# Performance work log

Measured on AMD Instinct MI355X. Metric: run time of the kernel, lower is better.

The kernel has to match this reference:

```python
import jax, jax.numpy as jnp
import numpy as np

N_HEAD = 16  # matches init_kwargs
LN_EPS = 1e-5


def setup_inputs() -> dict:
    key = jax.random.key(0)
    k0, k1, k2 = jax.random.split(key, 3)
    S, B, D = 2048, 2, 1024
    N, Dh = N_HEAD, D // N_HEAD
    h = jax.random.normal(k0, (S, B, D), dtype=jnp.float32)
    # causal mask, True = masked; source's dim==3 branch: shape [qlen, klen, batch]
    causal = jnp.triu(jnp.ones((S, S), dtype=bool), k=1)
    attn_mask = jnp.broadcast_to(causal[:, :, None], (S, S, B))
    W_qkv = jax.random.normal(k1, (D, 3 * N * Dh), dtype=jnp.float32) * (1.0 / np.sqrt(D))
    W_o = jax.random.normal(k2, (N * Dh, D), dtype=jnp.float32) * (1.0 / np.sqrt(N * Dh))
    gamma = jnp.ones((D,), dtype=jnp.float32)
    beta = jnp.zeros((D,), dtype=jnp.float32)
    return {"h": h, "attn_mask": attn_mask, "W_qkv": W_qkv, "W_o": W_o,
            "gamma": gamma, "beta": beta}


def reference(h, attn_mask, W_qkv, W_o, gamma, beta):
    # h: [S, B, D] (seq, batch, d_model) -- Transformer-XL layout
    S, B, D = h.shape
    N = N_HEAD
    Dh = W_o.shape[0] // N
    scale = 1.0 / np.sqrt(Dh)

    qkv = h @ W_qkv                                   # [S, B, 3*N*Dh]
    q, k, v = jnp.split(qkv, 3, axis=-1)
    q = q.reshape(S, B, N, Dh)
    k = k.reshape(S, B, N, Dh)
    v = v.reshape(S, B, N, Dh)

    # attention scores: [i, j, b, n]
    score = jnp.einsum('ibnd,jbnd->ijbn', q, k) * scale
    # mask (dim==3 branch of source): attn_mask [i, j, b] -> [i, j, b, 1]
    score = jnp.where(attn_mask[:, :, :, None], -jnp.inf, score)
    prob = jax.nn.softmax(score, axis=1)              # softmax over key axis j

    attn_vec = jnp.einsum('ijbn,jbnd->ibnd', prob, v).reshape(S, B, N * Dh)
    attn_out = attn_vec @ W_o                         # [S, B, D]

    # residual + LayerNorm (biased variance, like torch.nn.LayerNorm)
    x = h + attn_out
    mu = jnp.mean(x, axis=-1, keepdims=True)
    var = jnp.mean(jnp.square(x - mu), axis=-1, keepdims=True)
    out = (x - mu) * jax.lax.rsqrt(var + LN_EPS) * gamma + beta
    return out
```

## Files before the change

### kernel.cpp

```cpp
#include <hip/hip_runtime.h>

typedef unsigned short u16;
typedef unsigned int u32;
typedef __attribute__((ext_vector_type(8))) __bf16 bf16x8;
typedef __attribute__((ext_vector_type(4))) float f32x4;
typedef __attribute__((ext_vector_type(8))) unsigned short u16x8;
typedef __attribute__((ext_vector_type(4))) unsigned short u16x4;

__device__ __forceinline__ u16 f2bf(float f) {
    u32 u = __builtin_bit_cast(u32, f);
    u += 0x7fffu + ((u >> 16) & 1u);
    return (u16)(u >> 16);
}

__device__ __forceinline__ float fexp2(float x) {
#if __has_builtin(__builtin_amdgcn_exp2f)
    return __builtin_amdgcn_exp2f(x);
#else
    return exp2f(x);
#endif
}

__device__ __forceinline__ float frcp(float x) {
#if __has_builtin(__builtin_amdgcn_rcpf)
    return __builtin_amdgcn_rcpf(x);
#else
    return 1.0f / x;
#endif
}

__global__ __launch_bounds__(256) void conv_h_kernel(const float* __restrict__ h,
                                                     u16* __restrict__ hb) {
    int i = blockIdx.x * 256 + threadIdx.x;
    float4 v = ((const float4*)h)[i];
    u16x4 o = { f2bf(v.x), f2bf(v.y), f2bf(v.z), f2bf(v.w) };
    ((u16x4*)hb)[i] = o;
}

__global__ __launch_bounds__(256) void conv_wt_kernel(const float* __restrict__ W,
                                                      u16* __restrict__ Wt,
                                                      int R, int C,
                                                      int scale_rows, float scale) {
    __shared__ float tile[32][33];
    int t = threadIdx.x;
    int r = t >> 3, c4 = (t & 7) * 4;
    int gx = blockIdx.x * 32, gy = blockIdx.y * 32;
    float4 v = *(const float4*)&W[(size_t)(gy + r) * C + gx + c4];
    tile[r][c4 + 0] = v.x; tile[r][c4 + 1] = v.y;
    tile[r][c4 + 2] = v.z; tile[r][c4 + 3] = v.w;
    __syncthreads();
    float sc = (gx + r < scale_rows) ? scale : 1.0f;
    u16x4 o = { f2bf(tile[c4 + 0][r] * sc), f2bf(tile[c4 + 1][r] * sc),
                f2bf(tile[c4 + 2][r] * sc), f2bf(tile[c4 + 3][r] * sc) };
    *(u16x4*)&Wt[(size_t)(gx + r) * R + gy + c4] = o;
}

template <int MODE>
__global__ __launch_bounds__(256) void gemm_bt_kernel(
        const u16* __restrict__ A, const u16* __restrict__ Bt,
        u16* __restrict__ Cb, const float* __restrict__ H, float* __restrict__ X,
        int M, int N, int K) {
    constexpr int LDT = 40;
    __shared__ u16 alds[2][128 * LDT];
    __shared__ u16 blds[2][128 * LDT];
    const int t = threadIdx.x;
    const int lane = t & 63;
    const int wave = t >> 6;
    const int wm = wave >> 1, wn = wave & 1;
    const int m0 = blockIdx.x * 128;
    const int n0 = blockIdx.y * 128;
    const int nk = K >> 5;

    const int srow = t >> 1;
    const int sch = (t & 1) * 2;
    const u16* ga = A + (size_t)(m0 + srow) * K + sch * 8;
    const u16* gb = Bt + (size_t)(n0 + srow) * K + sch * 8;
    const int wo = srow * LDT + sch * 8;

    u16x8 ra0 = *(const u16x8*)(ga);
    u16x8 ra1 = *(const u16x8*)(ga + 8);
    u16x8 rb0 = *(const u16x8*)(gb);
    u16x8 rb1 = *(const u16x8*)(gb + 8);
    *(u16x8*)&alds[0][wo] = ra0;  *(u16x8*)&alds[0][wo + 8] = ra1;
    *(u16x8*)&blds[0][wo] = rb0;  *(u16x8*)&blds[0][wo + 8] = rb1;

    f32x4 acc[4][4] = {};
    const int ko = (lane >> 4) * 8;
    const int arow_base = wm * 64 + (lane & 15);
    const int brow_base = wn * 64 + (lane & 15);

    int cur = 0;
    for (int kt = 0; kt < nk; ++kt) {
        __syncthreads();
        if (kt + 1 < nk) {
            const u16* gan = ga + (kt + 1) * 32;
            const u16* gbn = gb + (kt + 1) * 32;
            ra0 = *(const u16x8*)(gan);
            ra1 = *(const u16x8*)(gan + 8);
            rb0 = *(const u16x8*)(gbn);
            rb1 = *(const u16x8*)(gbn + 8);
        }
        bf16x8 afrag[4], bfrag[4];
#pragma unroll
        for (int m = 0; m < 4; ++m)
            afrag[m] = *(const bf16x8*)&alds[cur][(arow_base + m * 16) * LDT + ko];
#pragma unroll
        for (int n = 0; n < 4; ++n)
            bfrag[n] = *(const bf16x8*)&blds[cur][(brow_base + n * 16) * LDT + ko];
#pragma unroll
        for (int m = 0; m < 4; ++m)
#pragma unroll
            for (int n = 0; n < 4; ++n)
                acc[m][n] = __builtin_amdgcn_mfma_f32_16x16x32_bf16(afrag[m], bfrag[n],
                                                                   acc[m][n], 0, 0, 0);
        if (kt + 1 < nk) {
            *(u16x8*)&alds[cur ^ 1][wo] = ra0;  *(u16x8*)&alds[cur ^ 1][wo + 8] = ra1;
            *(u16x8*)&blds[cur ^ 1][wo] = rb0;  *(u16x8*)&blds[cur ^ 1][wo + 8] = rb1;
        }
        cur ^= 1;
    }

#pragma unroll
    for (int m = 0; m < 4; ++m)
#pragma unroll
        for (int n = 0; n < 4; ++n)
#pragma unroll
            for (int r = 0; r < 4; ++r) {
                int row = m0 + wm * 64 + m * 16 + (lane >> 4) * 4 + r;
                int col = n0 + wn * 64 + n * 16 + (lane & 15);
                size_t idx = (size_t)row * N + col;
                if (MODE == 0) Cb[idx] = f2bf(acc[m][n][r]);
                else           X[idx] = acc[m][n][r] + H[idx];
            }
}

__global__ __launch_bounds__(256) void transpose_v_kernel(const u16* __restrict__ qkvb,
                                                          u16* __restrict__ vt) {
    __shared__ u16 tl[64][72];
    const int t = threadIdx.x;
    const int p = blockIdx.y;
    const int nn = p >> 1, b = p & 1;
    const int s0 = blockIdx.x * 64;
    const int r = t >> 2;
    const int ch = (t & 3) * 2;
    const u16* g = qkvb + ((size_t)(s0 + r) * 2 + b) * 3072 + 2048 + nn * 64;
    *(u16x8*)&tl[r][ch * 8]     = *(const u16x8*)(g + ch * 8);
    *(u16x8*)&tl[r][ch * 8 + 8] = *(const u16x8*)(g + ch * 8 + 8);
    __syncthreads();
    const int dh = t >> 2;
    const int sc = (t & 3) * 2;
    u16* o = vt + ((size_t)p * 64 + dh) * 2048 + s0;
#pragma unroll
    for (int q = 0; q < 2; ++q) {
        int scq = sc + q;
        u16x8 v;
#pragma unroll
        for (int j = 0; j < 8; ++j) v[j] = tl[scq * 8 + j][dh];
        *(u16x8*)(o + scq * 8) = v;
    }
}

__global__ __launch_bounds__(256) void attn_kernel(const u16* __restrict__ qkvb,
                                                   const u16* __restrict__ vt,
                                                   u16* __restrict__ attnb) {
    constexpr int LKT = 72;
    __shared__ u16 klds[64 * LKT];
    __shared__ u16 vlds[64 * LKT];
    __shared__ u16 plds[4][16 * LKT];
    const int t = threadIdx.x;
    const int lane = t & 63;
    const int w = t >> 6;
    const int bid = blockIdx.x;
    const int qt = 31 - (bid >> 5);
    const int p = bid & 31;
    const int nn = p >> 1, b = p & 1;
    const int i0 = qt * 64;

    const int li = lane & 15;
    const int lg = lane >> 4;

    const int qrow = i0 + w * 16 + li;
    const u16* qg = qkvb + ((size_t)qrow * 2 + b) * 3072 + nn * 64 + lg * 8;
    bf16x8 qa0 = *(const bf16x8*)(qg);
    bf16x8 qa1 = *(const bf16x8*)(qg + 32);

    f32x4 o[4] = {};
    float mrun = -3.0e38f;
    float lrun = 0.f;

    const int srow = t >> 2;
    const int sch = (t & 3) * 2;
    const u16* kg = qkvb + 1024 + nn * 64 + sch * 8;
    const u16* vg = vt + ((size_t)p * 64 + srow) * 2048 + sch * 8;

    const int nt = qt + 1;
    u16x8 k0, k1, v0, v1;
    {
        const u16* kgp = kg + ((size_t)srow * 2 + b) * 3072;
        k0 = *(const u16x8*)(kgp);  k1 = *(const u16x8*)(kgp + 8);
        v0 = *(const u16x8*)(vg);   v1 = *(const u16x8*)(vg + 8);
    }
    for (int jt = 0; jt < nt; ++jt) {
        const int j0 = jt * 64;
        __syncthreads();
        *(u16x8*)&klds[srow * LKT + sch * 8] = k0;
        *(u16x8*)&klds[srow * LKT + sch * 8 + 8] = k1;
        *(u16x8*)&vlds[srow * LKT + sch * 8] = v0;
        *(u16x8*)&vlds[srow * LKT + sch * 8 + 8] = v1;
        if (jt + 1 < nt) {
            const u16* kgp = kg + ((size_t)(j0 + 64 + srow) * 2 + b) * 3072;
            k0 = *(const u16x8*)(kgp);  k1 = *(const u16x8*)(kgp + 8);
            const u16* vgp = vg + j0 + 64;
            v0 = *(const u16x8*)(vgp);  v1 = *(const u16x8*)(vgp + 8);
        }
        __syncthreads();

        f32x4 st[4];
#pragma unroll
        for (int cf = 0; cf < 4; ++cf) {
            bf16x8 kb0 = *(const bf16x8*)&klds[(cf * 16 + li) * LKT + lg * 8];
            bf16x8 kb1 = *(const bf16x8*)&klds[(cf * 16 + li) * LKT + 32 + lg * 8];
            f32x4 z = {};
            z = __builtin_amdgcn_mfma_f32_16x16x32_bf16(kb0, qa0, z, 0, 0, 0);
            z = __builtin_amdgcn_mfma_f32_16x16x32_bf16(kb1, qa1, z, 0, 0, 0);
            st[cf] = z;
        }

        if (jt == qt) {
            const int it = w * 16 + li;
#pragma unroll
            for (int cf = 0; cf < 4; ++cf)
#pragma unroll
                for (int r = 0; r < 4; ++r) {
                    int jl = cf * 16 + lg * 4 + r;
                    if (jl > it) st[cf][r] = -3.0e38f;
                }
        }

        float mloc = st[0][0];
#pragma unroll
        for (int cf = 0; cf < 4; ++cf)
#pragma unroll
            for (int r = 0; r < 4; ++r) mloc = fmaxf(mloc, st[cf][r]);
        mloc = fmaxf(mloc, __shfl_xor(mloc, 16, 64));
        mloc = fmaxf(mloc, __shfl_xor(mloc, 32, 64));

        if (__any(mloc > mrun + 8.0f)) {
            float mnew = fmaxf(mrun, mloc);
            float alpha = fexp2(mrun - mnew);
            lrun *= alpha;
            mrun = mnew;
#pragma unroll
            for (int r = 0; r < 4; ++r) {
                float ar = __shfl(alpha, lg * 4 + r, 64);
#pragma unroll
                for (int cf = 0; cf < 4; ++cf) o[cf][r] *= ar;
            }
        }

        float rsum = 0.f;
#pragma unroll
        for (int cf = 0; cf < 4; ++cf) {
            u16x4 pw;
#pragma unroll
            for (int r = 0; r < 4; ++r) {
                float pv = fexp2(st[cf][r] - mrun);
                rsum += pv;
                pw[r] = f2bf(pv);
            }
            *(u16x4*)&plds[w][li * LKT + cf * 16 + lg * 4] = pw;
        }
        rsum += __shfl_xor(rsum, 16, 64);
        rsum += __shfl_xor(rsum, 32, 64);
        lrun += rsum;

        asm volatile("s_waitcnt lgkmcnt(0)" ::: "memory");
        __builtin_amdgcn_sched_barrier(0);

#pragma unroll
        for (int ks = 0; ks < 2; ++ks) {
            bf16x8 pa = *(const bf16x8*)&plds[w][li * LKT + ks * 32 + lg * 8];
#pragma unroll
            for (int cf = 0; cf < 4; ++cf) {
                bf16x8 vb = *(const bf16x8*)&vlds[(cf * 16 + li) * LKT + ks * 32 + lg * 8];
                o[cf] = __builtin_amdgcn_mfma_f32_16x16x32_bf16(pa, vb, o[cf], 0, 0, 0);
            }
        }
    }

    float rinv = frcp(lrun);
#pragma unroll
    for (int r = 0; r < 4; ++r) {
        float rv = __shfl(rinv, lg * 4 + r, 64);
        int srowg = i0 + w * 16 + lg * 4 + r;
        u16* og = attnb + ((size_t)srowg * 2 + b) * 1024 + nn * 64;
#pragma unroll
        for (int cf = 0; cf < 4; ++cf)
            og[cf * 16 + li] = f2bf(o[cf][r] * rv);
    }
}

__global__ __launch_bounds__(256) void ln_kernel(const float* __restrict__ X,
                                                 const float* __restrict__ gamma,
                                                 const float* __restrict__ beta,
                                                 float* __restrict__ out) {
    __shared__ float red[8];
    const int t = threadIdx.x;
    const int row = blockIdx.x;
    float4 v = ((const float4*)(X + (size_t)row * 1024))[t];
    float s = v.x + v.y + v.z + v.w;
#pragma unroll
    for (int off = 1; off < 64; off <<= 1) s += __shfl_xor(s, off, 64);
    if ((t & 63) == 0) red[t >> 6] = s;
    __syncthreads();
    float mu = (red[0] + red[1] + red[2] + red[3]) * (1.f / 1024.f);
    float dx = v.x - mu, dy = v.y - mu, dz = v.z - mu, dw = v.w - mu;
    float q = dx * dx + dy * dy + dz * dz + dw * dw;
#pragma unroll
    for (int off = 1; off < 64; off <<= 1) q += __shfl_xor(q, off, 64);
    if ((t & 63) == 0) red[4 + (t >> 6)] = q;
    __syncthreads();
    float var = (red[4] + red[5] + red[6] + red[7]) * (1.f / 1024.f);
    float rs = rsqrtf(var + 1e-5f);
    float4 g = ((const float4*)gamma)[t];
    float4 bt = ((const float4*)beta)[t];
    float4 o;
    o.x = dx * rs * g.x + bt.x;
    o.y = dy * rs * g.y + bt.y;
    o.z = dz * rs * g.z + bt.z;
    o.w = dw * rs * g.w + bt.w;
    ((float4*)(out + (size_t)row * 1024))[t] = o;
}

extern "C" void kernel_launch(void* const* d_in, const int* in_sizes, int n_in,
                              void* d_out, int out_size, void* d_ws, size_t ws_size,
                              hipStream_t stream) {
    const float* h     = (const float*)d_in[0];
    const float* Wqkv  = (const float*)d_in[2];
    const float* Wo    = (const float*)d_in[3];
    const float* gamma = (const float*)d_in[4];
    const float* beta  = (const float*)d_in[5];
    float* out = (float*)d_out;

    char* ws = (char*)d_ws;
    u16*   hb    = (u16*)(ws);
    u16*   wqkvt = (u16*)(ws + 8388608);
    u16*   wot   = (u16*)(ws + 14680064);
    u16*   qkvb  = (u16*)(ws + 16777216);
    u16*   vt    = (u16*)(ws + 41943040);
    u16*   attnb = (u16*)(ws + 50331648);
    float* xbuf  = (float*)(ws + 58720256);

    const float qscale = 0.125f * 1.44269504088896f;

    conv_h_kernel<<<4096, 256, 0, stream>>>(h, hb);
    conv_wt_kernel<<<dim3(96, 32), 256, 0, stream>>>(Wqkv, wqkvt, 1024, 3072, 1024, qscale);
    conv_wt_kernel<<<dim3(32, 32), 256, 0, stream>>>(Wo, wot, 1024, 1024, 0, 1.0f);
    gemm_bt_kernel<0><<<dim3(32, 24), 256, 0, stream>>>(hb, wqkvt, qkvb, nullptr, nullptr,
                                                        4096, 3072, 1024);
    transpose_v_kernel<<<dim3(32, 32), 256, 0, stream>>>(qkvb, vt);
    attn_kernel<<<1024, 256, 0, stream>>>(qkvb, vt, attnb);
    gemm_bt_kernel<1><<<dim3(32, 8), 256, 0, stream>>>(attnb, wot, nullptr, h, xbuf,
                                                       4096, 1024, 1024);
    ln_kernel<<<4096, 256, 0, stream>>>(xbuf, gamma, beta, out);
}
```

Before: 122.7 us.

## Use direct global-to-LDS loads in GEMM and 128-row query tiles in attention

The GEMM now stages A and B tiles with global_load_lds straight into unpadded shared memory, dropping the register round trip, with a wait and barrier after each k step. The attention kernel processes 128 query rows per block (two 16-row sub-blocks per wave), so each loaded K/V tile is reused twice as much, with half the grid and a reordered tile schedule. The work buys fewer LDS staging instructions and less K/V traffic, but costs unpadded LDS rows that may cause bank conflicts, more registers per wave, and fewer blocks in flight.

Result: slower. 132.5 us (+7.9%).

```diff
diff --git a/kernel.cpp b/kernel.cpp
--- a/kernel.cpp
+++ b/kernel.cpp
@@ -28,6 +28,10 @@
     return 1.0f / x;
 #endif
 }
+
+#define GLOAD_LDS16(gp, lp) __builtin_amdgcn_global_load_lds(                    \
+    (const __attribute__((address_space(1))) void*)(gp),                          \
+    (__attribute__((address_space(3))) void*)(lp), 16, 0, 0)
 
 __global__ __launch_bounds__(256) void conv_h_kernel(const float* __restrict__ h,
                                                      u16* __restrict__ hb) {
@@ -60,63 +64,62 @@
         const u16* __restrict__ A, const u16* __restrict__ Bt,
         u16* __restrict__ Cb, const float* __restrict__ H, float* __restrict__ X,
         int M, int N, int K) {
-    constexpr int LDT = 40;
-    __shared__ u16 alds[2][128 * LDT];
-    __shared__ u16 blds[2][128 * LDT];
+    __shared__ u16 alds[2][128 * 32];
+    __shared__ u16 blds[2][128 * 32];
     const int t = threadIdx.x;
     const int lane = t & 63;
     const int wave = t >> 6;
     const int wm = wave >> 1, wn = wave & 1;
+    const int li = lane & 15, lg = lane >> 4;
     const int m0 = blockIdx.x * 128;
     const int n0 = blockIdx.y * 128;
     const int nk = K >> 5;
 
-    const int srow = t >> 1;
-    const int sch = (t & 1) * 2;
-    const u16* ga = A + (size_t)(m0 + srow) * K + sch * 8;
-    const u16* gb = Bt + (size_t)(n0 + srow) * K + sch * 8;
-    const int wo = srow * LDT + sch * 8;
-
-    u16x8 ra0 = *(const u16x8*)(ga);
-    u16x8 ra1 = *(const u16x8*)(ga + 8);
-    u16x8 rb0 = *(const u16x8*)(gb);
-    u16x8 rb1 = *(const u16x8*)(gb + 8);
-    *(u16x8*)&alds[0][wo] = ra0;  *(u16x8*)&alds[0][wo + 8] = ra1;
-    *(u16x8*)&blds[0][wo] = rb0;  *(u16x8*)&blds[0][wo + 8] = rb1;
+    const int srow0 = (lane >> 2);
+    const int scol = (lane & 3) * 8;
+    const u16* gA = A + (size_t)(m0 + srow0) * K + scol;
+    const u16* gB = Bt + (size_t)(n0 + srow0) * K + scol;
+
+#define GEMM_STAGE(cur, kt)                                                      \
+    {                                                                            \
+        _Pragma("unroll")                                                        \
+        for (int jj = 0; jj < 2; ++jj) {                                         \
+            const int instr = wave * 2 + jj;                                     \
+            GLOAD_LDS16(gA + (size_t)(instr * 16) * K + (kt) * 32,               \
+                        &alds[cur][instr * 512]);                                \
+            GLOAD_LDS16(gB + (size_t)(instr * 16) * K + (kt) * 32,               \
+                        &blds[cur][instr * 512]);                                \
+        }                                                                        \
+    }
+
+    GEMM_STAGE(0, 0);
 
     f32x4 acc[4][4] = {};
-    const int ko = (lane >> 4) * 8;
-    const int arow_base = wm * 64 + (lane & 15);
-    const int brow_base = wn * 64 + (lane & 15);
+    const int ko = lg * 8;
+    const int arow_base = wm * 64 + li;
+    const int brow_base = wn * 64 + li;
+
+    asm volatile("s_waitcnt vmcnt(0)" ::: "memory");
+    __syncthreads();
 
     int cur = 0;
     for (int kt = 0; kt < nk; ++kt) {
-        __syncthreads();
-        if (kt + 1 < nk) {
-            const u16* gan = ga + (kt + 1) * 32;
-            const u16* gbn = gb + (kt + 1) * 32;
-            ra0 = *(const u16x8*)(gan);
-            ra1 = *(const u16x8*)(gan + 8);
-            rb0 = *(const u16x8*)(gbn);
-            rb1 = *(const u16x8*)(gbn + 8);
-        }
+        if (kt + 1 < nk) GEMM_STAGE(cur ^ 1, kt + 1);
         bf16x8 afrag[4], bfrag[4];
 #pragma unroll
         for (int m = 0; m < 4; ++m)
-            afrag[m] = *(const bf16x8*)&alds[cur][(arow_base + m * 16) * LDT + ko];
+            afrag[m] = *(const bf16x8*)&alds[cur][(arow_base + m * 16) * 32 + ko];
 #pragma unroll
         for (int n = 0; n < 4; ++n)
-            bfrag[n] = *(const bf16x8*)&blds[cur][(brow_base + n * 16) * LDT + ko];
+            bfrag[n] = *(const bf16x8*)&blds[cur][(brow_base + n * 16) * 32 + ko];
 #pragma unroll
         for (int m = 0; m < 4; ++m)
 #pragma unroll
             for (int n = 0; n < 4; ++n)
                 acc[m][n] = __builtin_amdgcn_mfma_f32_16x16x32_bf16(afrag[m], bfrag[n],
                                                                    acc[m][n], 0, 0, 0);
-        if (kt + 1 < nk) {
-            *(u16x8*)&alds[cur ^ 1][wo] = ra0;  *(u16x8*)&alds[cur ^ 1][wo + 8] = ra1;
-            *(u16x8*)&blds[cur ^ 1][wo] = rb0;  *(u16x8*)&blds[cur ^ 1][wo + 8] = rb1;
-        }
+        asm volatile("s_waitcnt vmcnt(0)" ::: "memory");
+        __syncthreads();
         cur ^= 1;
     }
 
@@ -126,8 +129,8 @@
         for (int n = 0; n < 4; ++n)
 #pragma unroll
             for (int r = 0; r < 4; ++r) {
-                int row = m0 + wm * 64 + m * 16 + (lane >> 4) * 4 + r;
-                int col = n0 + wn * 64 + n * 16 + (lane & 15);
+                int row = m0 + wm * 64 + m * 16 + lg * 4 + r;
+                int col = n0 + wn * 64 + n * 16 + li;
                 size_t idx = (size_t)row * N + col;
                 if (MODE == 0) Cb[idx] = f2bf(acc[m][n][r]);
                 else           X[idx] = acc[m][n][r] + H[idx];
@@ -166,34 +169,39 @@
     constexpr int LKT = 72;
     __shared__ u16 klds[64 * LKT];
     __shared__ u16 vlds[64 * LKT];
-    __shared__ u16 plds[4][16 * LKT];
+    __shared__ u16 plds[4][32 * LKT];
     const int t = threadIdx.x;
     const int lane = t & 63;
     const int w = t >> 6;
     const int bid = blockIdx.x;
-    const int qt = 31 - (bid >> 5);
+    const int g = bid >> 5;
+    const int qt = (g < 8) ? (15 - g) : (g - 8);
     const int p = bid & 31;
     const int nn = p >> 1, b = p & 1;
-    const int i0 = qt * 64;
+    const int i0 = qt * 128;
 
     const int li = lane & 15;
     const int lg = lane >> 4;
 
-    const int qrow = i0 + w * 16 + li;
-    const u16* qg = qkvb + ((size_t)qrow * 2 + b) * 3072 + nn * 64 + lg * 8;
-    bf16x8 qa0 = *(const bf16x8*)(qg);
-    bf16x8 qa1 = *(const bf16x8*)(qg + 32);
-
-    f32x4 o[4] = {};
-    float mrun = -3.0e38f;
-    float lrun = 0.f;
+    bf16x8 qa[2][2];
+#pragma unroll
+    for (int ib = 0; ib < 2; ++ib) {
+        const u16* qg = qkvb + ((size_t)(i0 + w * 32 + ib * 16 + li) * 2 + b) * 3072
+                        + nn * 64 + lg * 8;
+        qa[ib][0] = *(const bf16x8*)(qg);
+        qa[ib][1] = *(const bf16x8*)(qg + 32);
+    }
+
+    f32x4 o[4][2] = {};
+    float mrun[2] = { -3.0e38f, -3.0e38f };
+    float lrun[2] = { 0.f, 0.f };
 
     const int srow = t >> 2;
     const int sch = (t & 3) * 2;
     const u16* kg = qkvb + 1024 + nn * 64 + sch * 8;
     const u16* vg = vt + ((size_t)p * 64 + srow) * 2048 + sch * 8;
 
-    const int nt = qt + 1;
+    const int nt = 2 * qt + 2;
     u16x8 k0, k1, v0, v1;
     {
         const u16* kgp = kg + ((size_t)srow * 2 + b) * 3072;
@@ -215,89 +223,124 @@
         }
         __syncthreads();
 
-        f32x4 st[4];
-#pragma unroll
-        for (int cf = 0; cf < 4; ++cf) {
-            bf16x8 kb0 = *(const bf16x8*)&klds[(cf * 16 + li) * LKT + lg * 8];
-            bf16x8 kb1 = *(const bf16x8*)&klds[(cf * 16 + li) * LKT + 32 + lg * 8];
-            f32x4 z = {};
-            z = __builtin_amdgcn_mfma_f32_16x16x32_bf16(kb0, qa0, z, 0, 0, 0);
-            z = __builtin_amdgcn_mfma_f32_16x16x32_bf16(kb1, qa1, z, 0, 0, 0);
-            st[cf] = z;
+        const bool active = !(w < 2 && jt == nt - 1);
+        if (active) {
+            f32x4 st[4][2];
+#pragma unroll
+            for (int cf = 0; cf < 4; ++cf) {
+                bf16x8 kb0 = *(const bf16x8*)&klds[(cf * 16 + li) * LKT + lg * 8];
+                bf16x8 kb1 = *(const bf16x8*)&klds[(cf * 16 + li) * LKT + 32 + lg * 8];
+#pragma unroll
+                for (int ib = 0; ib < 2; ++ib) {
+                    f32x4 z = {};
+                    z = __builtin_amdgcn_mfma_f32_16x16x32_bf16(kb0, qa[ib][0], z, 0, 0, 0);
+                    z = __builtin_amdgcn_mfma_f32_16x16x32_bf16(kb1, qa[ib][1], z, 0, 0, 0);
+                    st[cf][ib] = z;
+                }
+            }
+
+            if (jt >= nt - 2) {
+#pragma unroll
+                for (int cf = 0; cf < 4; ++cf)
+#pragma unroll
+                    for (int ib = 0; ib < 2; ++ib) {
+                        const int igl = i0 + w * 32 + ib * 16 + li;
+#pragma unroll
+                        for (int r = 0; r < 4; ++r) {
+                            int jgl = j0 + cf * 16 + lg * 4 + r;
+                            if (jgl > igl) st[cf][ib][r] = -3.0e38f;
+                        }
+                    }
+            }
+
+            float mloc[2];
+#pragma unroll
+            for (int ib = 0; ib < 2; ++ib) {
+                float m = st[0][ib][0];
+#pragma unroll
+                for (int cf = 0; cf < 4; ++cf)
+#pragma unroll
+                    for (int r = 0; r < 4; ++r) m = fmaxf(m, st[cf][ib][r]);
+                m = fmaxf(m, __shfl_xor(m, 16, 64));
+                m = fmaxf(m, __shfl_xor(m, 32, 64));
+                mloc[ib] = m;
+            }
+
+            bool need = (mloc[0] > mrun[0] + 8.0f) || (mloc[1] > mrun[1] + 8.0f);
+            if (__any(need)) {
+                float alpha[2];
+#pragma unroll
+                for (int ib = 0; ib < 2; ++ib) {
+                    float mnew = fmaxf(mrun[ib], mloc[ib]);
+                    alpha[ib] = fexp2(mrun[ib] - mnew);
+                    lrun[ib] *= alpha[ib];
+                    mrun[ib] = mnew;
+                }
+#pragma unroll
+                for (int ib = 0; ib < 2; ++ib)
+#pragma unroll
+                    for (int r = 0; r < 4; ++r) {
+                        float ar = __shfl(alpha[ib], lg * 4 + r, 64);
+#pragma unroll
+                        for (int cf = 0; cf < 4; ++cf) o[cf][ib][r] *= ar;
+                    }
+            }
+
+            float rsum[2] = { 0.f, 0.f };
+#pragma unroll
+            for (int cf = 0; cf < 4; ++cf)
+#pragma unroll
+                for (int ib = 0; ib < 2; ++ib) {
+                    u16x4 pw;
+#pragma unroll
+                    for (int r = 0; r < 4; ++r) {
+                        float pv = fexp2(st[cf][ib][r] - mrun[ib]);
+                        rsum[ib] += pv;
+                        pw[r] = f2bf(pv);
+                    }
+                    *(u16x4*)&plds[w][(ib * 16 + li) * LKT + cf * 16 + lg * 4] = pw;
+                }
+#pragma unroll
+            for (int ib = 0; ib < 2; ++ib) {
+                float rs = rsum[ib];
+                rs += __shfl_xor(rs, 16, 64);
+                rs += __shfl_xor(rs, 32, 64);
+                lrun[ib] += rs;
+            }
+
+            asm volatile("s_waitcnt lgkmcnt(0)" ::: "memory");
+            __builtin_amdgcn_sched_barrier(0);
+
+#pragma unroll
+            for (int ks = 0; ks < 2; ++ks) {
+                bf16x8 pa[2];
+#pragma unroll
+                for (int ib = 0; ib < 2; ++ib)
+                    pa[ib] = *(const bf16x8*)&plds[w][(ib * 16 + li) * LKT + ks * 32 + lg * 8];
+#pragma unroll
+                for (int cf = 0; cf < 4; ++cf) {
+                    bf16x8 vb = *(const bf16x8*)&vlds[(cf * 16 + li) * LKT + ks * 32 + lg * 8];
+#pragma unroll
+                    for (int ib = 0; ib < 2; ++ib)
+                        o[cf][ib] = __builtin_amdgcn_mfma_f32_16x16x32_bf16(pa[ib], vb,
+                                                                            o[cf][ib], 0, 0, 0);
+                }
+            }
         }
-
-        if (jt == qt) {
-            const int it = w * 16 + li;
+    }
+
+    float rinv[2] = { frcp(lrun[0]), frcp(lrun[1]) };
+#pragma unroll
+    for (int ib = 0; ib < 2; ++ib)
+#pragma unroll
+        for (int r = 0; r < 4; ++r) {
+            float rv = __shfl(rinv[ib], lg * 4 + r, 64);
+            int row = i0 + w * 32 + ib * 16 + lg * 4 + r;
+            u16* og = attnb + ((size_t)row * 2 + b) * 1024 + nn * 64;
 #pragma unroll
             for (int cf = 0; cf < 4; ++cf)
-#pragma unroll
-                for (int r = 0; r < 4; ++r) {
-                    int jl = cf * 16 + lg * 4 + r;
-                    if (jl > it) st[cf][r] = -3.0e38f;
-                }
+                og[cf * 16 + li] = f2bf(o[cf][ib][r] * rv);
         }
-
-        float mloc = st[0][0];
-#pragma unroll
-        for (int cf = 0; cf < 4; ++cf)
-#pragma unroll
-            for (int r = 0; r < 4; ++r) mloc = fmaxf(mloc, st[cf][r]);
-        mloc = fmaxf(mloc, __shfl_xor(mloc, 16, 64));
-        mloc = fmaxf(mloc, __shfl_xor(mloc, 32, 64));
-
-        if (__any(mloc > mrun + 8.0f)) {
-            float mnew = fmaxf(mrun, mloc);
-            float alpha = fexp2(mrun - mnew);
-            lrun *= alpha;
-            mrun = mnew;
-#pragma unroll
-            for (int r = 0; r < 4; ++r) {
-                float ar = __shfl(alpha, lg * 4 + r, 64);
-#pragma unroll
-                for (int cf = 0; cf < 4; ++cf) o[cf][r] *= ar;
-            }
-        }
-
-        float rsum = 0.f;
-#pragma unroll
-        for (int cf = 0; cf < 4; ++cf) {
-            u16x4 pw;
-#pragma unroll
-            for (int r = 0; r < 4; ++r) {
-                float pv = fexp2(st[cf][r] - mrun);
-                rsum += pv;
-                pw[r] = f2bf(pv);
-            }
-            *(u16x4*)&plds[w][li * LKT + cf * 16 + lg * 4] = pw;
-        }
-        rsum += __shfl_xor(rsum, 16, 64);
-        rsum += __shfl_xor(rsum, 32, 64);
-        lrun += rsum;
-
-        asm volatile("s_waitcnt lgkmcnt(0)" ::: "memory");
-        __builtin_amdgcn_sched_barrier(0);
-
-#pragma unroll
-        for (int ks = 0; ks < 2; ++ks) {
-            bf16x8 pa = *(const bf16x8*)&plds[w][li * LKT + ks * 32 + lg * 8];
-#pragma unroll
-            for (int cf = 0; cf < 4; ++cf) {
-                bf16x8 vb = *(const bf16x8*)&vlds[(cf * 16 + li) * LKT + ks * 32 + lg * 8];
-                o[cf] = __builtin_amdgcn_mfma_f32_16x16x32_bf16(pa, vb, o[cf], 0, 0, 0);
-            }
-        }
-    }
-
-    float rinv = frcp(lrun);
-#pragma unroll
-    for (int r = 0; r < 4; ++r) {
-        float rv = __shfl(rinv, lg * 4 + r, 64);
-        int srowg = i0 + w * 16 + lg * 4 + r;
-        u16* og = attnb + ((size_t)srowg * 2 + b) * 1024 + nn * 64;
-#pragma unroll
-        for (int cf = 0; cf < 4; ++cf)
-            og[cf * 16 + li] = f2bf(o[cf][r] * rv);
-    }
 }
 
 __global__ __launch_bounds__(256) void ln_kernel(const float* __restrict__ X,
@@ -359,7 +402,7 @@
     gemm_bt_kernel<0><<<dim3(32, 24), 256, 0, stream>>>(hb, wqkvt, qkvb, nullptr, nullptr,
                                                         4096, 3072, 1024);
     transpose_v_kernel<<<dim3(32, 32), 256, 0, stream>>>(qkvb, vt);
-    attn_kernel<<<1024, 256, 0, stream>>>(qkvb, vt, attnb);
+    attn_kernel<<<512, 256, 0, stream>>>(qkvb, vt, attnb);
     gemm_bt_kernel<1><<<dim3(32, 8), 256, 0, stream>>>(attnb, wot, nullptr, h, xbuf,
                                                        4096, 1024, 1024);
     ln_kernel<<<4096, 256, 0, stream>>>(xbuf, gamma, beta, out);
```

## Double-buffer K/V in LDS, pass P via permlane swaps, rebalance tile order

Applied to the files above, without the earlier changes.

The attention loop now keeps two K/V buffers in shared memory, so there is one barrier per tile instead of two, and the next tile's LDS store happens after compute. When permlane32/16 swap builtins are available, softmax probabilities are packed with v_cvt_pk_bf16_f32 and rearranged across lanes by register permutes instead of a round trip through an LDS buffer. Block-to-query-tile mapping is reordered so long and short causal tiles are interleaved for better load balance, and s_setprio brackets the MFMA sections. The cost is doubled K/V LDS, and the permlane path depends on the compiler exposing those builtins.

Result: faster. 117.7 us (-4.1%).

```diff
diff --git a/kernel.cpp b/kernel.cpp
--- a/kernel.cpp
+++ b/kernel.cpp
@@ -6,6 +6,17 @@
 typedef __attribute__((ext_vector_type(4))) float f32x4;
 typedef __attribute__((ext_vector_type(8))) unsigned short u16x8;
 typedef __attribute__((ext_vector_type(4))) unsigned short u16x4;
+typedef __attribute__((ext_vector_type(2))) unsigned int u32x2;
+typedef __attribute__((ext_vector_type(4))) unsigned int u32x4;
+
+#if defined(__has_builtin)
+#if __has_builtin(__builtin_amdgcn_permlane32_swap) && __has_builtin(__builtin_amdgcn_permlane16_swap)
+#define USE_PERMLANE 1
+#endif
+#endif
+#ifndef USE_PERMLANE
+#define USE_PERMLANE 0
+#endif
 
 __device__ __forceinline__ u16 f2bf(float f) {
     u32 u = __builtin_bit_cast(u32, f);
@@ -164,14 +175,19 @@
                                                    const u16* __restrict__ vt,
                                                    u16* __restrict__ attnb) {
     constexpr int LKT = 72;
-    __shared__ u16 klds[64 * LKT];
-    __shared__ u16 vlds[64 * LKT];
+    __shared__ u16 klds[2][64 * LKT];
+    __shared__ u16 vlds[2][64 * LKT];
+#if !USE_PERMLANE
     __shared__ u16 plds[4][16 * LKT];
+#endif
     const int t = threadIdx.x;
     const int lane = t & 63;
     const int w = t >> 6;
     const int bid = blockIdx.x;
-    const int qt = 31 - (bid >> 5);
+    const int g = bid >> 5;
+    const int sq = g & 7, jq = g >> 3;
+    const int qt = (jq == 0) ? (31 - sq) : (jq == 1) ? (16 + sq)
+                 : (jq == 2) ? (15 - sq) : sq;
     const int p = bid & 31;
     const int nn = p >> 1, b = p & 1;
     const int i0 = qt * 64;
@@ -192,6 +208,7 @@
     const int sch = (t & 3) * 2;
     const u16* kg = qkvb + 1024 + nn * 64 + sch * 8;
     const u16* vg = vt + ((size_t)p * 64 + srow) * 2048 + sch * 8;
+    const int swo = srow * LKT + sch * 8;
 
     const int nt = qt + 1;
     u16x8 k0, k1, v0, v1;
@@ -200,31 +217,31 @@
         k0 = *(const u16x8*)(kgp);  k1 = *(const u16x8*)(kgp + 8);
         v0 = *(const u16x8*)(vg);   v1 = *(const u16x8*)(vg + 8);
     }
+    *(u16x8*)&klds[0][swo] = k0;  *(u16x8*)&klds[0][swo + 8] = k1;
+    *(u16x8*)&vlds[0][swo] = v0;  *(u16x8*)&vlds[0][swo + 8] = v1;
+    __syncthreads();
+
     for (int jt = 0; jt < nt; ++jt) {
-        const int j0 = jt * 64;
-        __syncthreads();
-        *(u16x8*)&klds[srow * LKT + sch * 8] = k0;
-        *(u16x8*)&klds[srow * LKT + sch * 8 + 8] = k1;
-        *(u16x8*)&vlds[srow * LKT + sch * 8] = v0;
-        *(u16x8*)&vlds[srow * LKT + sch * 8 + 8] = v1;
+        const int buf = jt & 1;
         if (jt + 1 < nt) {
-            const u16* kgp = kg + ((size_t)(j0 + 64 + srow) * 2 + b) * 3072;
+            const u16* kgp = kg + ((size_t)(jt * 64 + 64 + srow) * 2 + b) * 3072;
             k0 = *(const u16x8*)(kgp);  k1 = *(const u16x8*)(kgp + 8);
-            const u16* vgp = vg + j0 + 64;
+            const u16* vgp = vg + jt * 64 + 64;
             v0 = *(const u16x8*)(vgp);  v1 = *(const u16x8*)(vgp + 8);
         }
-        __syncthreads();
 
         f32x4 st[4];
+        __builtin_amdgcn_s_setprio(1);
 #pragma unroll
         for (int cf = 0; cf < 4; ++cf) {
-            bf16x8 kb0 = *(const bf16x8*)&klds[(cf * 16 + li) * LKT + lg * 8];
-            bf16x8 kb1 = *(const bf16x8*)&klds[(cf * 16 + li) * LKT + 32 + lg * 8];
+            bf16x8 kb0 = *(const bf16x8*)&klds[buf][(cf * 16 + li) * LKT + lg * 8];
+            bf16x8 kb1 = *(const bf16x8*)&klds[buf][(cf * 16 + li) * LKT + 32 + lg * 8];
             f32x4 z = {};
             z = __builtin_amdgcn_mfma_f32_16x16x32_bf16(kb0, qa0, z, 0, 0, 0);
             z = __builtin_amdgcn_mfma_f32_16x16x32_bf16(kb1, qa1, z, 0, 0, 0);
             st[cf] = z;
         }
+        __builtin_amdgcn_s_setprio(0);
 
         if (jt == qt) {
             const int it = w * 16 + li;
@@ -258,6 +275,41 @@
             }
         }
 
+#if USE_PERMLANE
+        float rsum = 0.f;
+        u32 wv[4][2];
+#pragma unroll
+        for (int cf = 0; cf < 4; ++cf)
+#pragma unroll
+            for (int rr = 0; rr < 2; ++rr) {
+                float p0 = fexp2(st[cf][2 * rr] - mrun);
+                float p1 = fexp2(st[cf][2 * rr + 1] - mrun);
+                rsum += p0 + p1;
+                u32 wres;
+                asm("v_cvt_pk_bf16_f32 %0, %1, %2" : "=v"(wres) : "v"(p0), "v"(p1));
+                wv[cf][rr] = wres;
+            }
+        rsum += __shfl_xor(rsum, 16, 64);
+        rsum += __shfl_xor(rsum, 32, 64);
+        lrun += rsum;
+
+        __builtin_amdgcn_s_setprio(1);
+#pragma unroll
+        for (int ks = 0; ks < 2; ++ks) {
+            u32x2 sa = __builtin_amdgcn_permlane32_swap(wv[2 * ks][0], wv[2 * ks + 1][0], false, false);
+            u32x2 fa = __builtin_amdgcn_permlane16_swap(sa[0], sa[1], false, false);
+            u32x2 sb = __builtin_amdgcn_permlane32_swap(wv[2 * ks][1], wv[2 * ks + 1][1], false, false);
+            u32x2 fb = __builtin_amdgcn_permlane16_swap(sb[0], sb[1], false, false);
+            u32x4 fw = { fa[0], fb[0], fa[1], fb[1] };
+            bf16x8 pa = __builtin_bit_cast(bf16x8, fw);
+#pragma unroll
+            for (int cf = 0; cf < 4; ++cf) {
+                bf16x8 vb = *(const bf16x8*)&vlds[buf][(cf * 16 + li) * LKT + ks * 32 + lg * 8];
+                o[cf] = __builtin_amdgcn_mfma_f32_16x16x32_bf16(pa, vb, o[cf], 0, 0, 0);
+            }
+        }
+        __builtin_amdgcn_s_setprio(0);
+#else
         float rsum = 0.f;
 #pragma unroll
         for (int cf = 0; cf < 4; ++cf) {
@@ -282,10 +334,17 @@
             bf16x8 pa = *(const bf16x8*)&plds[w][li * LKT + ks * 32 + lg * 8];
 #pragma unroll
             for (int cf = 0; cf < 4; ++cf) {
-                bf16x8 vb = *(const bf16x8*)&vlds[(cf * 16 + li) * LKT + ks * 32 + lg * 8];
+                bf16x8 vb = *(const bf16x8*)&vlds[buf][(cf * 16 + li) * LKT + ks * 32 + lg * 8];
                 o[cf] = __builtin_amdgcn_mfma_f32_16x16x32_bf16(pa, vb, o[cf], 0, 0, 0);
             }
         }
+#endif
+
+        if (jt + 1 < nt) {
+            *(u16x8*)&klds[buf ^ 1][swo] = k0;  *(u16x8*)&klds[buf ^ 1][swo + 8] = k1;
+            *(u16x8*)&vlds[buf ^ 1][swo] = v0;  *(u16x8*)&vlds[buf ^ 1][swo + 8] = v1;
+        }
+        __syncthreads();
     }
 
     float rinv = frcp(lrun);
```
